# Kernel optimization log

Hardware: AMD Instinct MI355X
Metric: run time of the kernel (lower is better)

Reference implementation:

```python
import jax, jax.numpy as jnp
import numpy as np

D_MODEL = 1024
H = 16
D = D_MODEL // H  # 64 per head
D_FF = 4096
LN_EPS = 1e-5


def layer_norm(x, gamma, beta):
    mu = jnp.mean(x, axis=-1, keepdims=True)
    var = jnp.mean(jnp.square(x - mu), axis=-1, keepdims=True)
    return (x - mu) * jax.lax.rsqrt(var + LN_EPS) * gamma + beta


def setup_inputs() -> dict:
    key = jax.random.key(0)
    ks = jax.random.split(key, 12)
    s = 1.0 / np.sqrt(D_MODEL)
    sf = 1.0 / np.sqrt(D_FF)
    return {
        "x": jax.random.normal(ks[0], (2, 2048, D_MODEL), jnp.float32),
        "src_mask": 0,
        "w_q": jax.random.normal(ks[1], (D_MODEL, D_MODEL), jnp.float32) * s,
        "w_k": jax.random.normal(ks[2], (D_MODEL, D_MODEL), jnp.float32) * s,
        "w_v": jax.random.normal(ks[3], (D_MODEL, D_MODEL), jnp.float32) * s,
        "w_0": jax.random.normal(ks[4], (D_MODEL, D_MODEL), jnp.float32) * s,
        "b_0": jnp.zeros((D_MODEL,), jnp.float32),
        "w_1": jax.random.normal(ks[5], (D_MODEL, D_FF), jnp.float32) * s,
        "b_1": jnp.zeros((D_FF,), jnp.float32),
        "w_2": jax.random.normal(ks[6], (D_FF, D_MODEL), jnp.float32) * sf,
        "b_2": jnp.zeros((D_MODEL,), jnp.float32),
        "g_1": jnp.ones((D_MODEL,), jnp.float32),
        "be_1": jnp.zeros((D_MODEL,), jnp.float32),
        "g_2": jnp.ones((D_MODEL,), jnp.float32),
        "be_2": jnp.zeros((D_MODEL,), jnp.float32),
    }


def reference(x, src_mask, w_q, w_k, w_v, w_0, b_0, w_1, b_1, w_2, b_2, g_1, be_1, g_2, be_2):
    N, S, _ = x.shape
    # --- pre-LN self-attention branch ---
    x_n = layer_norm(x, g_1, be_1)
    q = (x_n @ w_q).reshape(N, S, H, D).transpose(0, 2, 1, 3)  # [N,H,S,D]
    k = (x_n @ w_k).reshape(N, S, H, D).transpose(0, 2, 1, 3)
    v = (x_n @ w_v).reshape(N, S, H, D).transpose(0, 2, 1, 3)
    scores = jnp.einsum('nhqd,nhkd->nhqk', q, k) / np.sqrt(D)
    # src_mask == 0 (falsy) in the original -> no masking applied
    attn = jax.nn.softmax(scores, axis=-1)
    out = jnp.einsum('nhqk,nhkd->nhqd', attn, v)
    out = out.transpose(0, 2, 1, 3).reshape(N, S, H * D)
    attn_out = out @ w_0 + b_0
    x = x + attn_out  # dropout is identity in eval
    # --- pre-LN feedforward branch ---
    x_n = layer_norm(x, g_2, be_2)
    ff = jax.nn.relu(x_n @ w_1 + b_1) @ w_2 + b_2
    return x + ff
```

## Files before the change

### kernel.cpp

```cpp
#include <hip/hip_runtime.h>

typedef __bf16 bf16x8 __attribute__((ext_vector_type(8)));
typedef float f32x4 __attribute__((ext_vector_type(4)));
typedef unsigned short u16x8 __attribute__((ext_vector_type(8)));
typedef unsigned short u16x4 __attribute__((ext_vector_type(4)));

__device__ __forceinline__ unsigned short f2bf_bits(float f) {
  unsigned u = __float_as_uint(f);
  return (unsigned short)((u + 0x7FFFu + ((u >> 16) & 1u)) >> 16);
}

__device__ __forceinline__ float exp2_amd(float x) {
  return __builtin_amdgcn_exp2f(x);
}

__device__ __forceinline__ unsigned cvt_pk_bf16(float a, float b) {
  unsigned r;
  asm("v_cvt_pk_bf16_f32 %0, %1, %2" : "=v"(r) : "v"(a), "v"(b));
  return r;
}

__device__ __forceinline__ void gload16(const void* g, void* l) {
  __builtin_amdgcn_global_load_lds(
      (const __attribute__((address_space(1))) unsigned int*)g,
      (__attribute__((address_space(3))) unsigned int*)l, 16, 0, 0);
}

__global__ __launch_bounds__(256) void wconv_t(const float* __restrict__ src,
                                               unsigned short* __restrict__ dst,
                                               int R, int C) {
  __shared__ float tile[32][33];
  const int tx = threadIdx.x & 31, ty = threadIdx.x >> 5;
  const size_t c0 = (size_t)blockIdx.x * 32, r0 = (size_t)blockIdx.y * 32;
#pragma unroll
  for (int i = 0; i < 4; i++)
    tile[ty + i * 8][tx] = src[(r0 + ty + i * 8) * C + c0 + tx];
  __syncthreads();
#pragma unroll
  for (int i = 0; i < 4; i++) {
    int c = ty + i * 8;
    dst[(c0 + c) * R + r0 + tx] = f2bf_bits(tile[tx][c]);
  }
}

__global__ __launch_bounds__(256) void ln_k(const float* __restrict__ x,
                                            const float* __restrict__ g,
                                            const float* __restrict__ be,
                                            unsigned short* __restrict__ o) {
  const int row = blockIdx.x, tid = threadIdx.x;
  const float4 v = ((const float4*)(x + (size_t)row * 1024))[tid];
  float s = v.x + v.y + v.z + v.w;
  float s2 = v.x * v.x + v.y * v.y + v.z * v.z + v.w * v.w;
#pragma unroll
  for (int m = 1; m < 64; m <<= 1) {
    s += __shfl_xor(s, m);
    s2 += __shfl_xor(s2, m);
  }
  __shared__ float red[8];
  const int w = tid >> 6;
  if ((tid & 63) == 0) { red[w] = s; red[4 + w] = s2; }
  __syncthreads();
  s = red[0] + red[1] + red[2] + red[3];
  s2 = red[4] + red[5] + red[6] + red[7];
  const float mu = s * (1.f / 1024.f);
  const float rs_ = rsqrtf(s2 * (1.f / 1024.f) - mu * mu + 1e-5f);
  const float4 gg = ((const float4*)g)[tid];
  const float4 bb = ((const float4*)be)[tid];
  u16x4 pack;
  pack.x = f2bf_bits((v.x - mu) * rs_ * gg.x + bb.x);
  pack.y = f2bf_bits((v.y - mu) * rs_ * gg.y + bb.y);
  pack.z = f2bf_bits((v.z - mu) * rs_ * gg.z + bb.z);
  pack.w = f2bf_bits((v.w - mu) * rs_ * gg.w + bb.w);
  *(u16x4*)(o + (size_t)row * 1024 + tid * 4) = pack;
}

template <int EPI>
__global__ __launch_bounds__(256) void gemm_bt(
    const unsigned short* __restrict__ A, const unsigned short* __restrict__ Bt,
    const float* __restrict__ bias, const float* __restrict__ res,
    void* __restrict__ Cv, int M, int N, int K) {
  __shared__ __align__(16) unsigned short As[2][128 * 64];
  __shared__ __align__(16) unsigned short Bs[2][128 * 64];
  const int tid = threadIdx.x, lane = tid & 63, w = tid >> 6;
  const int lo = lane & 15, hi = lane >> 4;
  const int l8 = lane >> 3, l7 = lane & 7;
  const int scol = ((l7 ^ l8) << 3);
  const int nwg = gridDim.x * gridDim.y;
  int bid = blockIdx.y * gridDim.x + blockIdx.x;
  if ((nwg & 7) == 0) bid = (bid & 7) * (nwg >> 3) + (bid >> 3);
  const int bx = bid % gridDim.x, by = bid / gridDim.x;
  const size_t rowBase = (size_t)by * 128;
  const size_t colBase = (size_t)bx * 128;
  f32x4 acc[4][4];
#pragma unroll
  for (int i = 0; i < 4; i++)
#pragma unroll
    for (int j = 0; j < 4; j++) acc[i][j] = (f32x4){0.f, 0.f, 0.f, 0.f};
  const int wr = (w >> 1) * 64, wc = (w & 1) * 64;
  const unsigned short* aSrc = A + (rowBase + (size_t)w * 32 + l8) * K + scol;
  const unsigned short* bSrc = Bt + (colBase + (size_t)w * 32 + l8) * K + scol;

  const int NT = K >> 6;
  auto stage = [&](int t, int buf) {
    const int kb = t << 6;
#pragma unroll
    for (int c = 0; c < 4; c++) {
      gload16(aSrc + (size_t)c * 8 * K + kb, &As[buf][(w * 4 + c) * 512]);
      gload16(bSrc + (size_t)c * 8 * K + kb, &Bs[buf][(w * 4 + c) * 512]);
    }
  };

  stage(0, 0);
  stage(1, 1);
  asm volatile("s_waitcnt vmcnt(8)" ::: "memory");
  __builtin_amdgcn_s_barrier();

  for (int t = 0; t < NT; ++t) {
    const int cur = t & 1;
    const char* asb = (const char*)As[cur];
    const char* bsb = (const char*)Bs[cur];
    __builtin_amdgcn_s_setprio(1);
#pragma unroll
    for (int ks = 0; ks < 2; ks++) {
      bf16x8 af[4], bfr[4];
      const int kbyte = ks * 64 + (hi << 4);
#pragma unroll
      for (int i = 0; i < 4; i++) {
        const int ar = wr + i * 16 + lo;
        af[i] = *(const bf16x8*)(asb + ar * 128 + (kbyte ^ ((ar & 7) << 4)));
        const int br = wc + i * 16 + lo;
        bfr[i] = *(const bf16x8*)(bsb + br * 128 + (kbyte ^ ((br & 7) << 4)));
      }
#pragma unroll
      for (int i = 0; i < 4; i++)
#pragma unroll
        for (int j = 0; j < 4; j++)
          acc[i][j] = __builtin_amdgcn_mfma_f32_16x16x32_bf16(af[i], bfr[j], acc[i][j], 0, 0, 0);
    }
    __builtin_amdgcn_s_setprio(0);
    asm volatile("s_waitcnt lgkmcnt(0)" ::: "memory");
    __builtin_amdgcn_s_barrier();
    if (t + 2 < NT) {
      stage(t + 2, cur);
      asm volatile("s_waitcnt vmcnt(8)" ::: "memory");
    } else {
      asm volatile("s_waitcnt vmcnt(0)" ::: "memory");
    }
    __builtin_amdgcn_s_barrier();
  }

#pragma unroll
  for (int i = 0; i < 4; i++) {
#pragma unroll
    for (int r = 0; r < 4; r++) {
      const size_t row = rowBase + wr + i * 16 + hi * 4 + r;
#pragma unroll
      for (int j = 0; j < 4; j++) {
        const size_t col = colBase + wc + j * 16 + lo;
        float v = acc[i][j][r];
        if (EPI >= 1) v += bias[col];
        if (EPI == 1) {
          ((float*)Cv)[row * N + col] = v + res[row * N + col];
        } else if (EPI == 2) {
          ((unsigned short*)Cv)[row * N + col] = f2bf_bits(fmaxf(v, 0.f));
        } else {
          ((unsigned short*)Cv)[row * N + col] = f2bf_bits(v);
        }
      }
    }
  }
}

__global__ __launch_bounds__(256) void attn_k(const unsigned short* __restrict__ Q,
                                              const unsigned short* __restrict__ K,
                                              const unsigned short* __restrict__ V,
                                              unsigned short* __restrict__ O) {
  __shared__ __align__(16) unsigned short Ks[2][64 * 64];
  __shared__ __align__(16) unsigned short Vt[2][64 * 64];
  const int tid = threadIdx.x, lane = tid & 63, w = tid >> 6;
  const int lo = lane & 15, hi = lane >> 4;
  const int l8 = lane >> 3, l7 = lane & 7;
  const int scol = ((l7 ^ l8) << 3);
  const int h = blockIdx.y, n = blockIdx.z;
  const size_t tRow0 = (size_t)n * 2048;
  const int colBase = h * 64;
  const int LD = 3072;
  const float SC = 0.125f * 1.44269504f;

  const unsigned short* qrow = Q + (tRow0 + blockIdx.x * 64 + w * 16 + lo) * LD + colBase;
  const bf16x8 qf0 = *(const bf16x8*)(qrow + hi * 8);
  const bf16x8 qf1 = *(const bf16x8*)(qrow + 32 + hi * 8);
  float m2 = -1e30f, l_r = 0.f;
  f32x4 oacc[4];
#pragma unroll
  for (int d = 0; d < 4; d++) oacc[d] = (f32x4){0.f, 0.f, 0.f, 0.f};

  const int vkv = tid & 63, vdg = tid >> 6;
  const unsigned short* vbase = V + (tRow0 + vkv) * LD + colBase + vdg * 16;
  const unsigned short* kbase = K + (tRow0 + (size_t)w * 16 + l8) * LD + colBase + scol;

  u16x8 v0 = *(const u16x8*)(vbase);
  u16x8 v1 = *(const u16x8*)(vbase + 8);
#pragma unroll
  for (int c = 0; c < 2; c++)
    gload16(kbase + (size_t)c * 8 * LD, &Ks[0][(w * 2 + c) * 512]);
  {
    char* vt = (char*)Vt[0];
#pragma unroll
    for (int j = 0; j < 8; j++) {
      *(unsigned short*)(vt + (vdg * 16 + j) * 128 + ((vkv * 2) ^ (j << 4))) = v0[j];
      *(unsigned short*)(vt + (vdg * 16 + 8 + j) * 128 + ((vkv * 2) ^ (j << 4))) = v1[j];
    }
  }
  __syncthreads();

  for (int t = 0; t < 32; ++t) {
    const int cur = t & 1;
    if (t < 31) {
      v0 = *(const u16x8*)(vbase + (size_t)(t + 1) * 64 * LD);
      v1 = *(const u16x8*)(vbase + (size_t)(t + 1) * 64 * LD + 8);
#pragma unroll
      for (int c = 0; c < 2; c++)
        gload16(kbase + ((size_t)(t + 1) * 64 + c * 8) * LD, &Ks[cur ^ 1][(w * 2 + c) * 512]);
    }
    f32x4 s[4];
    const char* ksb = (const char*)Ks[cur];
    __builtin_amdgcn_s_setprio(1);
#pragma unroll
    for (int f = 0; f < 4; f++) {
      const int kr = f * 16 + lo;
      const bf16x8 b0 = *(const bf16x8*)(ksb + kr * 128 + ((hi * 16) ^ ((kr & 7) << 4)));
      const bf16x8 b1 = *(const bf16x8*)(ksb + kr * 128 + ((64 + hi * 16) ^ ((kr & 7) << 4)));
      s[f] = __builtin_amdgcn_mfma_f32_16x16x32_bf16(b0, qf0, (f32x4){0.f, 0.f, 0.f, 0.f}, 0, 0, 0);
      s[f] = __builtin_amdgcn_mfma_f32_16x16x32_bf16(b1, qf1, s[f], 0, 0, 0);
    }
    __builtin_amdgcn_s_setprio(0);
    float mx = fmaxf(fmaxf(fmaxf(s[0][0], s[0][1]), fmaxf(s[0][2], s[0][3])),
                     fmaxf(fmaxf(s[1][0], s[1][1]), fmaxf(s[1][2], s[1][3])));
    mx = fmaxf(mx, fmaxf(fmaxf(fmaxf(s[2][0], s[2][1]), fmaxf(s[2][2], s[2][3])),
                         fmaxf(fmaxf(s[3][0], s[3][1]), fmaxf(s[3][2], s[3][3]))));
    mx = fmaxf(mx, __shfl_xor(mx, 16));
    mx = fmaxf(mx, __shfl_xor(mx, 32));
    const float mx2v = mx * SC;
    if (__any(mx2v > m2 + 8.f)) {
      const float mn = fmaxf(m2, mx2v);
      const float al = exp2_amd(m2 - mn);
      l_r *= al;
      m2 = mn;
#pragma unroll
      for (int r = 0; r < 4; r++) {
        const float alr = __shfl(al, hi * 4 + r);
#pragma unroll
        for (int d = 0; d < 4; d++) oacc[d][r] *= alr;
      }
    }
    float p[4][4];
    float lsum = 0.f;
#pragma unroll
    for (int f = 0; f < 4; f++)
#pragma unroll
      for (int r = 0; r < 4; r++) {
        p[f][r] = exp2_amd(fmaf(s[f][r], SC, -m2));
        lsum += p[f][r];
      }
    l_r += lsum;
    unsigned W2[4][2];
#pragma unroll
    for (int f = 0; f < 4; f++) {
      W2[f][0] = cvt_pk_bf16(p[f][0], p[f][1]);
      W2[f][1] = cvt_pk_bf16(p[f][2], p[f][3]);
    }
    __builtin_amdgcn_s_setprio(1);
#pragma unroll
    for (int ks = 0; ks < 2; ks++) {
      unsigned wa[2], wb[2];
#pragma unroll
      for (int hh = 0; hh < 2; hh++) {
        unsigned X = W2[ks * 2][hh], Y = W2[ks * 2 + 1][hh];
        asm("v_permlane32_swap_b32 %0, %1" : "+v"(X), "+v"(Y));
        const unsigned Bx = __shfl_xor((int)Y, 16);
        const unsigned Ax = __shfl_xor((int)X, 16);
        wa[hh] = (hi & 1) ? Bx : X;
        wb[hh] = (hi & 1) ? Y : Ax;
      }
      union { unsigned u[4]; bf16x8 v; } apu;
      apu.u[0] = wa[0]; apu.u[1] = wa[1]; apu.u[2] = wb[0]; apu.u[3] = wb[1];
      const int kbyte = ks * 64 + (hi << 4);
#pragma unroll
      for (int d = 0; d < 4; d++) {
        const int dr = d * 16 + lo;
        const bf16x8 bv = *(const bf16x8*)((const char*)Vt[cur] + dr * 128 + (kbyte ^ ((dr & 7) << 4)));
        oacc[d] = __builtin_amdgcn_mfma_f32_16x16x32_bf16(apu.v, bv, oacc[d], 0, 0, 0);
      }
    }
    __builtin_amdgcn_s_setprio(0);
    if (t < 31) {
      char* vt = (char*)Vt[cur ^ 1];
#pragma unroll
      for (int j = 0; j < 8; j++) {
        *(unsigned short*)(vt + (vdg * 16 + j) * 128 + ((vkv * 2) ^ (j << 4))) = v0[j];
        *(unsigned short*)(vt + (vdg * 16 + 8 + j) * 128 + ((vkv * 2) ^ (j << 4))) = v1[j];
      }
    }
    __syncthreads();
  }
  float l = l_r;
  l += __shfl_xor(l, 16);
  l += __shfl_xor(l, 32);
  const float inv = 1.f / l;
#pragma unroll
  for (int r = 0; r < 4; r++) {
    const float invr = __shfl(inv, hi * 4 + r);
    const size_t row = tRow0 + blockIdx.x * 64 + w * 16 + hi * 4 + r;
#pragma unroll
    for (int d = 0; d < 4; d++)
      O[row * 1024 + colBase + d * 16 + lo] = f2bf_bits(oacc[d][r] * invr);
  }
}

extern "C" void kernel_launch(void* const* d_in, const int* in_sizes, int n_in,
                              void* d_out, int out_size, void* d_ws, size_t ws_size,
                              hipStream_t stream) {
  (void)in_sizes; (void)n_in; (void)out_size; (void)ws_size;
  const float* x   = (const float*)d_in[0];
  const float* w_q = (const float*)d_in[2];
  const float* w_k = (const float*)d_in[3];
  const float* w_v = (const float*)d_in[4];
  const float* w_0 = (const float*)d_in[5];
  const float* b_0 = (const float*)d_in[6];
  const float* w_1 = (const float*)d_in[7];
  const float* b_1 = (const float*)d_in[8];
  const float* w_2 = (const float*)d_in[9];
  const float* b_2 = (const float*)d_in[10];
  const float* g_1 = (const float*)d_in[11];
  const float* be_1 = (const float*)d_in[12];
  const float* g_2 = (const float*)d_in[13];
  const float* be_2 = (const float*)d_in[14];

  char* ws = (char*)d_ws;
  size_t off = 0;
  auto alloc = [&](size_t bytes) {
    void* p = ws + off;
    off += (bytes + 255) & ~(size_t)255;
    return p;
  };
  const size_t MB = 1024 * 1024;
  unsigned short* wt_q = (unsigned short*)alloc(2 * MB);
  unsigned short* wt_k = (unsigned short*)alloc(2 * MB);
  unsigned short* wt_v = (unsigned short*)alloc(2 * MB);
  unsigned short* wt_0 = (unsigned short*)alloc(2 * MB);
  unsigned short* wt_1 = (unsigned short*)alloc(8 * MB);
  unsigned short* wt_2 = (unsigned short*)alloc(8 * MB);
  unsigned short* xn   = (unsigned short*)alloc(8 * MB);
  unsigned short* qkv  = (unsigned short*)alloc(24 * MB);
  unsigned short* aO   = (unsigned short*)alloc(8 * MB);
  float*          x1f  = (float*)alloc(16 * MB);
  unsigned short* ff1  = (unsigned short*)alloc(32 * MB);

  wconv_t<<<dim3(32, 32), 256, 0, stream>>>(w_q, wt_q, 1024, 1024);
  wconv_t<<<dim3(32, 32), 256, 0, stream>>>(w_k, wt_k, 1024, 1024);
  wconv_t<<<dim3(32, 32), 256, 0, stream>>>(w_v, wt_v, 1024, 1024);
  wconv_t<<<dim3(32, 32), 256, 0, stream>>>(w_0, wt_0, 1024, 1024);
  wconv_t<<<dim3(128, 32), 256, 0, stream>>>(w_1, wt_1, 1024, 4096);
  wconv_t<<<dim3(32, 128), 256, 0, stream>>>(w_2, wt_2, 4096, 1024);

  ln_k<<<4096, 256, 0, stream>>>(x, g_1, be_1, xn);
  gemm_bt<0><<<dim3(24, 32), 256, 0, stream>>>(xn, wt_q, nullptr, nullptr, qkv, 4096, 3072, 1024);
  attn_k<<<dim3(32, 16, 2), 256, 0, stream>>>(qkv, qkv + 1024, qkv + 2048, aO);
  gemm_bt<1><<<dim3(8, 32), 256, 0, stream>>>(aO, wt_0, b_0, x, x1f, 4096, 1024, 1024);
  ln_k<<<4096, 256, 0, stream>>>(x1f, g_2, be_2, xn);
  gemm_bt<2><<<dim3(32, 32), 256, 0, stream>>>(xn, wt_1, b_1, nullptr, ff1, 4096, 4096, 1024);
  gemm_bt<1><<<dim3(8, 32), 256, 0, stream>>>(ff1, wt_2, b_2, x1f, (float*)d_out, 4096, 1024, 4096);
}
```

Baseline: 284.8 us.

## Split-K the FF2 GEMM with bf16 partials and add attention V-transpose and permlane reductions

The FF2 GEMM (K=4096, only 256 workgroups) is split four ways along K, so 1024 workgroups can fill the GPU. Each split writes bf16 partial sums into the reused qkv buffer, and a separate reduction kernel adds bias and residual. In attention, the V transpose into LDS now uses 8-byte loads with byte-perm packing instead of scalar 2-byte stores, and the cross-lane max and sum reductions use permlane swaps instead of shuffles. Rounding the partials to bf16 adds some precision loss, and the partials cost extra global traffic plus one more kernel launch.

```diff
diff --git a/kernel.cpp b/kernel.cpp
--- a/kernel.cpp
+++ b/kernel.cpp
@@ -18,6 +18,27 @@
   unsigned r;
   asm("v_cvt_pk_bf16_f32 %0, %1, %2" : "=v"(r) : "v"(a), "v"(b));
   return r;
+}
+
+__device__ __forceinline__ float red16_max(float x) {
+  unsigned a = __float_as_uint(x), b = a;
+  asm("v_permlane16_swap_b32 %0, %1" : "+v"(a), "+v"(b));
+  return fmaxf(__uint_as_float(a), __uint_as_float(b));
+}
+__device__ __forceinline__ float red32_max(float x) {
+  unsigned a = __float_as_uint(x), b = a;
+  asm("v_permlane32_swap_b32 %0, %1" : "+v"(a), "+v"(b));
+  return fmaxf(__uint_as_float(a), __uint_as_float(b));
+}
+__device__ __forceinline__ float red16_sum(float x) {
+  unsigned a = __float_as_uint(x), b = a;
+  asm("v_permlane16_swap_b32 %0, %1" : "+v"(a), "+v"(b));
+  return __uint_as_float(a) + __uint_as_float(b);
+}
+__device__ __forceinline__ float red32_sum(float x) {
+  unsigned a = __float_as_uint(x), b = a;
+  asm("v_permlane32_swap_b32 %0, %1" : "+v"(a), "+v"(b));
+  return __uint_as_float(a) + __uint_as_float(b);
 }
 
 __device__ __forceinline__ void gload16(const void* g, void* l) {
@@ -78,7 +99,7 @@
 __global__ __launch_bounds__(256) void gemm_bt(
     const unsigned short* __restrict__ A, const unsigned short* __restrict__ Bt,
     const float* __restrict__ bias, const float* __restrict__ res,
-    void* __restrict__ Cv, int M, int N, int K) {
+    void* __restrict__ Cv, int M, int N, int K, int KL) {
   __shared__ __align__(16) unsigned short As[2][128 * 64];
   __shared__ __align__(16) unsigned short Bs[2][128 * 64];
   const int tid = threadIdx.x, lane = tid & 63, w = tid >> 6;
@@ -91,16 +112,17 @@
   const int bx = bid % gridDim.x, by = bid / gridDim.x;
   const size_t rowBase = (size_t)by * 128;
   const size_t colBase = (size_t)bx * 128;
+  const int kOff = blockIdx.z * KL;
   f32x4 acc[4][4];
 #pragma unroll
   for (int i = 0; i < 4; i++)
 #pragma unroll
     for (int j = 0; j < 4; j++) acc[i][j] = (f32x4){0.f, 0.f, 0.f, 0.f};
   const int wr = (w >> 1) * 64, wc = (w & 1) * 64;
-  const unsigned short* aSrc = A + (rowBase + (size_t)w * 32 + l8) * K + scol;
-  const unsigned short* bSrc = Bt + (colBase + (size_t)w * 32 + l8) * K + scol;
-
-  const int NT = K >> 6;
+  const unsigned short* aSrc = A + (rowBase + (size_t)w * 32 + l8) * K + scol + kOff;
+  const unsigned short* bSrc = Bt + (colBase + (size_t)w * 32 + l8) * K + scol + kOff;
+
+  const int NT = KL >> 6;
   auto stage = [&](int t, int buf) {
     const int kb = t << 6;
 #pragma unroll
@@ -149,6 +171,7 @@
     __builtin_amdgcn_s_barrier();
   }
 
+  const size_t zOff = (size_t)blockIdx.z * M * N;
 #pragma unroll
   for (int i = 0; i < 4; i++) {
 #pragma unroll
@@ -158,17 +181,42 @@
       for (int j = 0; j < 4; j++) {
         const size_t col = colBase + wc + j * 16 + lo;
         float v = acc[i][j][r];
-        if (EPI >= 1) v += bias[col];
         if (EPI == 1) {
-          ((float*)Cv)[row * N + col] = v + res[row * N + col];
+          ((float*)Cv)[row * N + col] = v + bias[col] + res[row * N + col];
         } else if (EPI == 2) {
-          ((unsigned short*)Cv)[row * N + col] = f2bf_bits(fmaxf(v, 0.f));
+          ((unsigned short*)Cv)[row * N + col] = f2bf_bits(fmaxf(v + bias[col], 0.f));
+        } else if (EPI == 3) {
+          ((unsigned short*)Cv)[zOff + row * N + col] = f2bf_bits(v);
         } else {
           ((unsigned short*)Cv)[row * N + col] = f2bf_bits(v);
         }
       }
     }
   }
+}
+
+__global__ __launch_bounds__(256) void ff2red(const unsigned short* __restrict__ p,
+                                              const float* __restrict__ bias,
+                                              const float* __restrict__ res,
+                                              float* __restrict__ out) {
+  const size_t i = ((size_t)blockIdx.x * 256 + threadIdx.x) * 8;
+  const int col = (int)(i & 1023);
+  const float4 b0 = *(const float4*)(bias + col);
+  const float4 b1 = *(const float4*)(bias + col + 4);
+  const float4 r0 = *(const float4*)(res + i);
+  const float4 r1 = *(const float4*)(res + i + 4);
+  float acc[8] = {b0.x + r0.x, b0.y + r0.y, b0.z + r0.z, b0.w + r0.w,
+                  b1.x + r1.x, b1.y + r1.y, b1.z + r1.z, b1.w + r1.w};
+#pragma unroll
+  for (int z = 0; z < 4; z++) {
+    const u16x8 pv = *(const u16x8*)(p + (size_t)z * 4194304 + i);
+#pragma unroll
+    for (int j = 0; j < 8; j++) acc[j] += __uint_as_float((unsigned)pv[j] << 16);
+  }
+  float4 o0 = {acc[0], acc[1], acc[2], acc[3]};
+  float4 o1 = {acc[4], acc[5], acc[6], acc[7]};
+  *(float4*)(out + i) = o0;
+  *(float4*)(out + i + 4) = o1;
 }
 
 __global__ __launch_bounds__(256) void attn_k(const unsigned short* __restrict__ Q,
@@ -195,30 +243,44 @@
 #pragma unroll
   for (int d = 0; d < 4; d++) oacc[d] = (f32x4){0.f, 0.f, 0.f, 0.f};
 
-  const int vkv = tid & 63, vdg = tid >> 6;
-  const unsigned short* vbase = V + (tRow0 + vkv) * LD + colBase + vdg * 16;
+  const int kvg = tid >> 4, dgi = tid & 15;
+  const unsigned short* vsrc = V + (tRow0 + (size_t)kvg * 4) * LD + colBase + dgi * 4;
   const unsigned short* kbase = K + (tRow0 + (size_t)w * 16 + l8) * LD + colBase + scol;
 
-  u16x8 v0 = *(const u16x8*)(vbase);
-  u16x8 v1 = *(const u16x8*)(vbase + 8);
+  auto vwrite = [&](char* vt, uint2 R0, uint2 R1, uint2 R2, uint2 R3) {
+#pragma unroll
+    for (int j = 0; j < 4; j++) {
+      const unsigned sel = (j & 1) ? 0x03020706u : 0x01000504u;
+      const unsigned s0 = (j >= 2) ? R0.y : R0.x;
+      const unsigned s1 = (j >= 2) ? R1.y : R1.x;
+      const unsigned s2 = (j >= 2) ? R2.y : R2.x;
+      const unsigned s3 = (j >= 2) ? R3.y : R3.x;
+      uint2 cw;
+      cw.x = __builtin_amdgcn_perm(s0, s1, sel);
+      cw.y = __builtin_amdgcn_perm(s2, s3, sel);
+      const int d = dgi * 4 + j;
+      *(uint2*)(vt + d * 128 + ((kvg * 8) ^ ((d & 7) << 4))) = cw;
+    }
+  };
+
+  uint2 R0 = *(const uint2*)(vsrc);
+  uint2 R1 = *(const uint2*)(vsrc + LD);
+  uint2 R2 = *(const uint2*)(vsrc + 2 * LD);
+  uint2 R3 = *(const uint2*)(vsrc + 3 * LD);
 #pragma unroll
   for (int c = 0; c < 2; c++)
     gload16(kbase + (size_t)c * 8 * LD, &Ks[0][(w * 2 + c) * 512]);
-  {
-    char* vt = (char*)Vt[0];
-#pragma unroll
-    for (int j = 0; j < 8; j++) {
-      *(unsigned short*)(vt + (vdg * 16 + j) * 128 + ((vkv * 2) ^ (j << 4))) = v0[j];
-      *(unsigned short*)(vt + (vdg * 16 + 8 + j) * 128 + ((vkv * 2) ^ (j << 4))) = v1[j];
-    }
-  }
+  vwrite((char*)Vt[0], R0, R1, R2, R3);
   __syncthreads();
 
   for (int t = 0; t < 32; ++t) {
     const int cur = t & 1;
     if (t < 31) {
-      v0 = *(const u16x8*)(vbase + (size_t)(t + 1) * 64 * LD);
-      v1 = *(const u16x8*)(vbase + (size_t)(t + 1) * 64 * LD + 8);
+      const unsigned short* vs = vsrc + (size_t)(t + 1) * 64 * LD;
+      R0 = *(const uint2*)(vs);
+      R1 = *(const uint2*)(vs + LD);
+      R2 = *(const uint2*)(vs + 2 * LD);
+      R3 = *(const uint2*)(vs + 3 * LD);
 #pragma unroll
       for (int c = 0; c < 2; c++)
         gload16(kbase + ((size_t)(t + 1) * 64 + c * 8) * LD, &Ks[cur ^ 1][(w * 2 + c) * 512]);
@@ -239,8 +301,8 @@
                      fmaxf(fmaxf(s[1][0], s[1][1]), fmaxf(s[1][2], s[1][3])));
     mx = fmaxf(mx, fmaxf(fmaxf(fmaxf(s[2][0], s[2][1]), fmaxf(s[2][2], s[2][3])),
                          fmaxf(fmaxf(s[3][0], s[3][1]), fmaxf(s[3][2], s[3][3]))));
-    mx = fmaxf(mx, __shfl_xor(mx, 16));
-    mx = fmaxf(mx, __shfl_xor(mx, 32));
+    mx = red16_max(mx);
+    mx = red32_max(mx);
     const float mx2v = mx * SC;
     if (__any(mx2v > m2 + 8.f)) {
       const float mn = fmaxf(m2, mx2v);
@@ -294,19 +356,10 @@
       }
     }
     __builtin_amdgcn_s_setprio(0);
-    if (t < 31) {
-      char* vt = (char*)Vt[cur ^ 1];
-#pragma unroll
-      for (int j = 0; j < 8; j++) {
-        *(unsigned short*)(vt + (vdg * 16 + j) * 128 + ((vkv * 2) ^ (j << 4))) = v0[j];
-        *(unsigned short*)(vt + (vdg * 16 + 8 + j) * 128 + ((vkv * 2) ^ (j << 4))) = v1[j];
-      }
-    }
+    if (t < 31) vwrite((char*)Vt[cur ^ 1], R0, R1, R2, R3);
     __syncthreads();
   }
-  float l = l_r;
-  l += __shfl_xor(l, 16);
-  l += __shfl_xor(l, 32);
+  float l = red32_sum(red16_sum(l_r));
   const float inv = 1.f / l;
 #pragma unroll
   for (int r = 0; r < 4; r++) {
@@ -356,6 +409,7 @@
   unsigned short* aO   = (unsigned short*)alloc(8 * MB);
   float*          x1f  = (float*)alloc(16 * MB);
   unsigned short* ff1  = (unsigned short*)alloc(32 * MB);
+  unsigned short* part = qkv;
 
   wconv_t<<<dim3(32, 32), 256, 0, stream>>>(w_q, wt_q, 1024, 1024);
   wconv_t<<<dim3(32, 32), 256, 0, stream>>>(w_k, wt_k, 1024, 1024);
@@ -365,10 +419,11 @@
   wconv_t<<<dim3(32, 128), 256, 0, stream>>>(w_2, wt_2, 4096, 1024);
 
   ln_k<<<4096, 256, 0, stream>>>(x, g_1, be_1, xn);
-  gemm_bt<0><<<dim3(24, 32), 256, 0, stream>>>(xn, wt_q, nullptr, nullptr, qkv, 4096, 3072, 1024);
+  gemm_bt<0><<<dim3(24, 32), 256, 0, stream>>>(xn, wt_q, nullptr, nullptr, qkv, 4096, 3072, 1024, 1024);
   attn_k<<<dim3(32, 16, 2), 256, 0, stream>>>(qkv, qkv + 1024, qkv + 2048, aO);
-  gemm_bt<1><<<dim3(8, 32), 256, 0, stream>>>(aO, wt_0, b_0, x, x1f, 4096, 1024, 1024);
+  gemm_bt<1><<<dim3(8, 32), 256, 0, stream>>>(aO, wt_0, b_0, x, x1f, 4096, 1024, 1024, 1024);
   ln_k<<<4096, 256, 0, stream>>>(x1f, g_2, be_2, xn);
-  gemm_bt<2><<<dim3(32, 32), 256, 0, stream>>>(xn, wt_1, b_1, nullptr, ff1, 4096, 4096, 1024);
-  gemm_bt<1><<<dim3(8, 32), 256, 0, stream>>>(ff1, wt_2, b_2, x1f, (float*)d_out, 4096, 1024, 4096);
-}
+  gemm_bt<2><<<dim3(32, 32), 256, 0, stream>>>(xn, wt_1, b_1, nullptr, ff1, 4096, 4096, 1024, 1024);
+  gemm_bt<3><<<dim3(8, 32, 4), 256, 0, stream>>>(ff1, wt_2, nullptr, nullptr, part, 4096, 1024, 4096, 1024);
+  ff2red<<<2048, 256, 0, stream>>>(part, b_2, x1f, (float*)d_out);
+}
```

Measured after the change: 274.0 us. 3.8% less time.
